# Kernel tuning notes

Measured on AMD Instinct MI355X. Metric: run time of the kernel, lower is better.

## Reference

```python
import jax, jax.numpy as jnp
import numpy as np

EPS_S = 1e-06
EPS_R = 1e-06

def _gaussian_masks(mu, logsx, logsy, rho, H, W, dtype):
    # coordinate grid in [-1,1], grid[h,w] = (x, y)
    ys = jnp.linspace(-1.0, 1.0, H, dtype=dtype)
    xs = jnp.linspace(-1.0, 1.0, W, dtype=dtype)
    Y, X = jnp.meshgrid(ys, xs, indexing='ij')  # [H,W]
    sx = jnp.exp(logsx)[:, None, None] + EPS_S   # [n,1,1]
    sy = jnp.exp(logsy)[:, None, None] + EPS_S
    r = jnp.tanh(rho)[:, None, None]
    xc = (X[None] - mu[:, 0, None, None]) / sx   # [n,H,W]
    yc = (Y[None] - mu[:, 1, None, None]) / sy
    A = xc ** 2 + yc ** 2 - 2.0 * r * xc * yc
    denom = 2.0 * (1.0 - r ** 2 + EPS_R)
    return jnp.exp(-A / denom)                   # [n,H,W]

def setup_inputs() -> dict:
    key = jax.random.key(0)
    ks = jax.random.split(key, 6)
    B, C, H, W, n = 32, 256, 36, 64, 4096
    feat = jax.random.normal(ks[0], (B, C, H, W), dtype=jnp.float32)
    mu = jax.random.uniform(ks[1], (n, 2), dtype=jnp.float32) * 2.0 - 1.0
    logsx = jnp.zeros((n,), dtype=jnp.float32)
    logsy = jnp.zeros((n,), dtype=jnp.float32)
    rho = jnp.zeros((n,), dtype=jnp.float32)
    weight = jax.random.normal(ks[5], (n, C), dtype=jnp.float32) * 0.01
    return {"feat": feat, "mu": mu, "logsx": logsx, "logsy": logsy, "rho": rho, "weight": weight}

def reference(feat, mu, logsx, logsy, rho, weight):
    B, C, H, W = feat.shape
    G = _gaussian_masks(mu, logsx, logsy, rho, H, W, feat.dtype)  # [n,H,W]
    # pooled[b,n,c] = sum_{h,w} feat[b,c,h,w] * G[n,h,w]  (batched GEMM)
    pooled = jnp.einsum('bchw,nhw->bnc', feat, G)
    out = jnp.einsum('bnc,nc->bn', pooled, weight.astype(feat.dtype))
    return out
```

## Files before the change

kernel.cpp:

```cpp
#include <hip/hip_runtime.h>
#include <hip/hip_bf16.h>

#define P_HW   2304
#define NG     4096
#define NCOL   8192
#define KDIM   P_HW
#define NT     72

typedef __bf16 bf16x8 __attribute__((ext_vector_type(8)));
typedef float  f32x4  __attribute__((ext_vector_type(4)));

__device__ __forceinline__ unsigned short f2bf(float f) {
    union { float f; unsigned int u; } x; x.f = f;
    unsigned int r = x.u + 0x7FFFu + ((x.u >> 16) & 1u);
    return (unsigned short)(r >> 16);
}

__global__ __launch_bounds__(256) void prep_kernel(
    const float* __restrict__ feat,
    const float* __restrict__ mu,
    const float* __restrict__ logsx,
    const float* __restrict__ logsy,
    const float* __restrict__ rho,
    unsigned short* __restrict__ F,
    unsigned short* __restrict__ G,
    float* __restrict__ out) {
    const int bid = blockIdx.x;
    const int tid = threadIdx.x;
    if (bid < 9216) {
        const size_t i = ((size_t)bid * 256 + tid) * 8;
        const float4 v0 = *(const float4*)(feat + i);
        const float4 v1 = *(const float4*)(feat + i + 4);
        union { unsigned short s[8]; uint4 q; } o;
        o.s[0] = f2bf(v0.x); o.s[1] = f2bf(v0.y); o.s[2] = f2bf(v0.z); o.s[3] = f2bf(v0.w);
        o.s[4] = f2bf(v1.x); o.s[5] = f2bf(v1.y); o.s[6] = f2bf(v1.z); o.s[7] = f2bf(v1.w);
        *(uint4*)(F + i) = o.q;
    } else if (bid < 13312) {
        const int n = bid - 9216;
        const float mux = mu[2 * n], muy = mu[2 * n + 1];
        const float sx = __expf(logsx[n]) + 1e-6f;
        const float sy = __expf(logsy[n]) + 1e-6f;
        const float r  = tanhf(rho[n]);
        const float inv_den = 1.0f / (2.0f * (1.0f - r * r + 1e-6f));
        const float isx = 1.0f / sx, isy = 1.0f / sy;
        for (int base = tid * 8; base < P_HW; base += 2048) {
            const int h = base >> 6, w0 = base & 63;
            const float Y  = -1.0f + (float)h * (2.0f / 35.0f);
            const float yc = (Y - muy) * isy;
            union { unsigned short s[8]; uint4 q; } o;
#pragma unroll
            for (int j = 0; j < 8; ++j) {
                const float X  = -1.0f + (float)(w0 + j) * (2.0f / 63.0f);
                const float xc = (X - mux) * isx;
                const float A  = xc * xc + yc * yc - 2.0f * r * xc * yc;
                o.s[j] = f2bf(__expf(-A * inv_den));
            }
            *(uint4*)&G[(size_t)n * P_HW + base] = o.q;
        }
    } else {
        const size_t i = ((size_t)(bid - 13312) * 256 + tid) * 8;
        const float4 z = {0.f, 0.f, 0.f, 0.f};
        *(float4*)(out + i)     = z;
        *(float4*)(out + i + 4) = z;
    }
}

__device__ __forceinline__ void async16(const void* g, void* l) {
    __builtin_amdgcn_global_load_lds(
        (__attribute__((address_space(1))) void*)(unsigned long long)g,
        (__attribute__((address_space(3))) void*)(unsigned int)(unsigned long long)l,
        16, 0, 0);
}

__global__ __launch_bounds__(512, 2) void gemm_fused(
    const unsigned short* __restrict__ G,
    const unsigned short* __restrict__ F,
    const float* __restrict__ weight,
    float* __restrict__ out)
{
    __shared__ __align__(16) unsigned short lds[4 * 16384];

    const int tid  = threadIdx.x;
    const int lane = tid & 63;
    const int wid  = tid >> 6;
    const int wr   = wid >> 2;
    const int wc   = wid & 3;
    const int quad = lane >> 4, m = lane & 15;

    const int rowBase = blockIdx.y * 256;
    const int colBase = blockIdx.x * 256;

    const int rA = tid >> 2;
    const int cA = (tid & 3) ^ ((tid >> 3) & 3);
    const unsigned short* pA = G + (size_t)(rowBase + rA) * KDIM + cA * 8;
    const unsigned short* pB = F + (size_t)(colBase + rA) * KDIM + cA * 8;

    const int sw   = (quad ^ ((m >> 1) & 3)) * 8;
    const int aoff = (wr * 128 + m) * 32 + sw;
    const int boff = (wc * 64  + m) * 32 + sw;

    f32x4 acc[8][4];
#pragma unroll
    for (int i = 0; i < 8; ++i)
#pragma unroll
        for (int j = 0; j < 4; ++j)
            acc[i][j] = (f32x4){0.f, 0.f, 0.f, 0.f};

#pragma unroll
    for (int t = 0; t < 3; ++t) {
        const int bo = t * 16384;
#pragma unroll
        for (int i = 0; i < 2; ++i)
            async16(pA + t * 32 + i * (128 * KDIM), &lds[bo + i * 4096 + tid * 8]);
#pragma unroll
        for (int i = 0; i < 2; ++i)
            async16(pB + t * 32 + i * (128 * KDIM), &lds[bo + 8192 + i * 4096 + tid * 8]);
    }
    asm volatile("s_waitcnt vmcnt(8)" ::: "memory");
    __builtin_amdgcn_s_barrier();

    for (int t = 0; t < NT; ++t) {
        const int bo  = (t & 3) * 16384;
        const int w   = (t + 3 >= NT) ? (t + 3 - NT) : (t + 3);
        const int wbo = (w & 3) * 16384;
        const unsigned short* pAw = pA + w * 32;
        const unsigned short* pBw = pB + w * 32;

        bf16x8 a[4], b[4];
#pragma unroll
        for (int i = 0; i < 4; ++i)
            a[i] = *(const bf16x8*)&lds[bo + aoff + i * 512];
#pragma unroll
        for (int j = 0; j < 4; ++j)
            b[j] = *(const bf16x8*)&lds[bo + 8192 + boff + j * 512];
#pragma unroll
        for (int i = 0; i < 2; ++i)
            async16(pAw + i * (128 * KDIM), &lds[wbo + i * 4096 + tid * 8]);
        __builtin_amdgcn_sched_barrier(0);
        __builtin_amdgcn_s_barrier();
        asm volatile("s_waitcnt lgkmcnt(0)" ::: "memory");
        __builtin_amdgcn_sched_barrier(0);
        __builtin_amdgcn_s_setprio(1);
#pragma unroll
        for (int i = 0; i < 4; ++i)
#pragma unroll
            for (int j = 0; j < 4; ++j)
                acc[i][j] = __builtin_amdgcn_mfma_f32_16x16x32_bf16(a[i], b[j], acc[i][j], 0, 0, 0);
        __builtin_amdgcn_s_setprio(0);
        __builtin_amdgcn_sched_barrier(0);
        __builtin_amdgcn_s_barrier();
        __builtin_amdgcn_sched_barrier(0);
#pragma unroll
        for (int i = 0; i < 4; ++i)
            a[i] = *(const bf16x8*)&lds[bo + aoff + (i + 4) * 512];
#pragma unroll
        for (int i = 0; i < 2; ++i)
            async16(pBw + i * (128 * KDIM), &lds[wbo + 8192 + i * 4096 + tid * 8]);
        __builtin_amdgcn_sched_barrier(0);
        __builtin_amdgcn_s_barrier();
        asm volatile("s_waitcnt lgkmcnt(0)" ::: "memory");
        __builtin_amdgcn_sched_barrier(0);
        __builtin_amdgcn_s_setprio(1);
#pragma unroll
        for (int i = 0; i < 4; ++i)
#pragma unroll
            for (int j = 0; j < 4; ++j)
                acc[i + 4][j] = __builtin_amdgcn_mfma_f32_16x16x32_bf16(a[i], b[j], acc[i + 4][j], 0, 0, 0);
        __builtin_amdgcn_s_setprio(0);
        asm volatile("s_waitcnt vmcnt(8)" ::: "memory");
        __builtin_amdgcn_sched_barrier(0);
        __builtin_amdgcn_s_barrier();
        __builtin_amdgcn_sched_barrier(0);
    }

    asm volatile("s_waitcnt vmcnt(0)" ::: "memory");
    __syncthreads();

    float* red = (float*)lds;
    const int cwbase = wc * 64 + m;
#pragma unroll
    for (int i = 0; i < 8; ++i) {
#pragma unroll
        for (int reg = 0; reg < 4; ++reg) {
            const int nloc = wr * 128 + i * 16 + quad * 4 + reg;
            const float* wrow = weight + (size_t)(rowBase + nloc) * 256 + cwbase;
            float s = 0.f;
#pragma unroll
            for (int j = 0; j < 4; ++j)
                s += acc[i][j][reg] * wrow[j * 16];
            s += __shfl_xor(s, 1);
            s += __shfl_xor(s, 2);
            s += __shfl_xor(s, 4);
            s += __shfl_xor(s, 8);
            if (m == 0)
                red[wc * 256 + nloc] = s;
        }
    }
    __syncthreads();
    if (tid < 256) {
        const float s = red[tid] + red[256 + tid] + red[512 + tid] + red[768 + tid];
        out[(size_t)blockIdx.x * NG + rowBase + tid] = s;
    }
}

extern "C" void kernel_launch(void* const* d_in, const int* in_sizes, int n_in,
                              void* d_out, int out_size, void* d_ws, size_t ws_size,
                              hipStream_t stream) {
    const float* feat   = (const float*)d_in[0];
    const float* mu     = (const float*)d_in[1];
    const float* logsx  = (const float*)d_in[2];
    const float* logsy  = (const float*)d_in[3];
    const float* rho    = (const float*)d_in[4];
    const float* weight = (const float*)d_in[5];
    float* out = (float*)d_out;

    unsigned short* Gbuf = (unsigned short*)d_ws;
    unsigned short* Fbuf = Gbuf + (size_t)NG * P_HW;

    hipLaunchKernelGGL(prep_kernel, dim3(13376), dim3(256), 0, stream,
                       feat, mu, logsx, logsy, rho, Fbuf, Gbuf, out);

    hipLaunchKernelGGL(gemm_fused, dim3(NCOL / 256, NG / 256), dim3(512), 0, stream,
                       Gbuf, Fbuf, weight, out);
}
```

Measured before the change: 271.6 us.

## Unroll GEMM main loop by four and use one barrier per K-step

Rewrites the main K loop of the fused GEMM. It is unrolled by four so the LDS ring-buffer offsets become compile-time constants. All four async global-to-LDS loads for a stage are issued at the top of each step, all eight A fragments are read at once, and the three barrier/wait phases per step become a single vmcnt wait plus one barrier. This cuts barrier and scheduling overhead and gives the compiler freedom to interleave LDS reads with MFMAs. The cost is higher register pressure and the loss of the explicit sched_barrier ordering.

```diff
diff --git a/kernel.cpp b/kernel.cpp
--- a/kernel.cpp
+++ b/kernel.cpp
@@ -109,68 +109,51 @@
 #pragma unroll
     for (int t = 0; t < 3; ++t) {
         const int bo = t * 16384;
-#pragma unroll
-        for (int i = 0; i < 2; ++i)
-            async16(pA + t * 32 + i * (128 * KDIM), &lds[bo + i * 4096 + tid * 8]);
-#pragma unroll
-        for (int i = 0; i < 2; ++i)
-            async16(pB + t * 32 + i * (128 * KDIM), &lds[bo + 8192 + i * 4096 + tid * 8]);
+        async16(pA + t * 32,                  &lds[bo + tid * 8]);
+        async16(pA + t * 32 + 128 * KDIM,     &lds[bo + 4096 + tid * 8]);
+        async16(pB + t * 32,                  &lds[bo + 8192 + tid * 8]);
+        async16(pB + t * 32 + 128 * KDIM,     &lds[bo + 12288 + tid * 8]);
     }
     asm volatile("s_waitcnt vmcnt(8)" ::: "memory");
     __builtin_amdgcn_s_barrier();
-
-    for (int t = 0; t < NT; ++t) {
-        const int bo  = (t & 3) * 16384;
-        const int w   = (t + 3 >= NT) ? (t + 3 - NT) : (t + 3);
-        const int wbo = (w & 3) * 16384;
-        const unsigned short* pAw = pA + w * 32;
-        const unsigned short* pBw = pB + w * 32;
-
-        bf16x8 a[4], b[4];
-#pragma unroll
-        for (int i = 0; i < 4; ++i)
-            a[i] = *(const bf16x8*)&lds[bo + aoff + i * 512];
-#pragma unroll
-        for (int j = 0; j < 4; ++j)
-            b[j] = *(const bf16x8*)&lds[bo + 8192 + boff + j * 512];
-#pragma unroll
-        for (int i = 0; i < 2; ++i)
-            async16(pAw + i * (128 * KDIM), &lds[wbo + i * 4096 + tid * 8]);
-        __builtin_amdgcn_sched_barrier(0);
-        __builtin_amdgcn_s_barrier();
-        asm volatile("s_waitcnt lgkmcnt(0)" ::: "memory");
-        __builtin_amdgcn_sched_barrier(0);
-        __builtin_amdgcn_s_setprio(1);
-#pragma unroll
-        for (int i = 0; i < 4; ++i)
+    asm volatile("" ::: "memory");
+
+    for (int tt = 0; tt < NT; tt += 4) {
+#pragma unroll
+        for (int u = 0; u < 4; ++u) {
+            const int t   = tt + u;
+            const int bo  = u * 16384;
+            const int wbo = ((u + 3) & 3) * 16384;
+            int w = t + 3;
+            if (w >= NT) w -= NT;
+            const unsigned short* pAw = pA + w * 32;
+            const unsigned short* pBw = pB + w * 32;
+
+            async16(pAw,              &lds[wbo + tid * 8]);
+            async16(pAw + 128 * KDIM, &lds[wbo + 4096 + tid * 8]);
+            async16(pBw,              &lds[wbo + 8192 + tid * 8]);
+            async16(pBw + 128 * KDIM, &lds[wbo + 12288 + tid * 8]);
+
+            bf16x8 a[8], b[4];
 #pragma unroll
             for (int j = 0; j < 4; ++j)
-                acc[i][j] = __builtin_amdgcn_mfma_f32_16x16x32_bf16(a[i], b[j], acc[i][j], 0, 0, 0);
-        __builtin_amdgcn_s_setprio(0);
-        __builtin_amdgcn_sched_barrier(0);
-        __builtin_amdgcn_s_barrier();
-        __builtin_amdgcn_sched_barrier(0);
-#pragma unroll
-        for (int i = 0; i < 4; ++i)
-            a[i] = *(const bf16x8*)&lds[bo + aoff + (i + 4) * 512];
-#pragma unroll
-        for (int i = 0; i < 2; ++i)
-            async16(pBw + i * (128 * KDIM), &lds[wbo + 8192 + i * 4096 + tid * 8]);
-        __builtin_amdgcn_sched_barrier(0);
-        __builtin_amdgcn_s_barrier();
-        asm volatile("s_waitcnt lgkmcnt(0)" ::: "memory");
-        __builtin_amdgcn_sched_barrier(0);
-        __builtin_amdgcn_s_setprio(1);
-#pragma unroll
-        for (int i = 0; i < 4; ++i)
-#pragma unroll
-            for (int j = 0; j < 4; ++j)
-                acc[i + 4][j] = __builtin_amdgcn_mfma_f32_16x16x32_bf16(a[i], b[j], acc[i + 4][j], 0, 0, 0);
-        __builtin_amdgcn_s_setprio(0);
-        asm volatile("s_waitcnt vmcnt(8)" ::: "memory");
-        __builtin_amdgcn_sched_barrier(0);
-        __builtin_amdgcn_s_barrier();
-        __builtin_amdgcn_sched_barrier(0);
+                b[j] = *(const bf16x8*)&lds[bo + 8192 + boff + j * 512];
+#pragma unroll
+            for (int i = 0; i < 8; ++i)
+                a[i] = *(const bf16x8*)&lds[bo + aoff + i * 512];
+
+            __builtin_amdgcn_s_setprio(1);
+#pragma unroll
+            for (int i = 0; i < 8; ++i)
+#pragma unroll
+                for (int j = 0; j < 4; ++j)
+                    acc[i][j] = __builtin_amdgcn_mfma_f32_16x16x32_bf16(a[i], b[j], acc[i][j], 0, 0, 0);
+            __builtin_amdgcn_s_setprio(0);
+
+            asm volatile("s_waitcnt vmcnt(8)" ::: "memory");
+            __builtin_amdgcn_s_barrier();
+            asm volatile("" ::: "memory");
+        }
     }
 
     asm volatile("s_waitcnt vmcnt(0)" ::: "memory");
```

Result: no change. 270.3 us (-0.5%).
